# Kernel tuning notes

Measured on AMD Instinct MI355X. Metric: run time of the kernel, lower is better.

The kernel has to match this reference:

```python
import jax, jax.numpy as jnp
import numpy as np

B, T, C, H = 2, 2048, 1024, 16
R = 32
LORA_SCALE = 0.5  # lora_alpha / r = (0.5*rank) / rank
HD = C // H


def setup_inputs() -> dict:
    key = jax.random.key(0)
    ks = jax.random.split(key, 8)
    std = 0.02
    return {
        "x": jax.random.normal(ks[0], (B, T, C), jnp.float32),
        "w_attn": jax.random.normal(ks[1], (3 * C, C), jnp.float32) * std,
        "b_attn": jnp.zeros((3 * C,), jnp.float32),
        "la_attn": jax.random.normal(ks[2], (R, C), jnp.float32) * std,
        "lb_attn": jax.random.normal(ks[3], (3 * C, R), jnp.float32) * std,
        "w_proj": jax.random.normal(ks[4], (C, C), jnp.float32) * std,
        "b_proj": jnp.zeros((C,), jnp.float32),
        "la_proj": jax.random.normal(ks[5], (R, C), jnp.float32) * std,
        "lb_proj": jax.random.normal(ks[6], (C, R), jnp.float32) * std,
    }


def lora_linear(x, w, b, la, lb):
    # y = x @ W^T + b + scale * (x @ A^T) @ B^T
    return x @ w.T + b + LORA_SCALE * ((x @ la.T) @ lb.T)


def reference(x, w_attn, b_attn, la_attn, lb_attn, w_proj, b_proj, la_proj, lb_proj):
    Bsz, Tlen, Cdim = x.shape
    qkv = lora_linear(x, w_attn, b_attn, la_attn, lb_attn)  # [B,T,3C]
    q, k, v = jnp.split(qkv, 3, axis=2)
    # [B,T,C] -> [B,H,T,hd]
    rs = lambda t: t.reshape(Bsz, Tlen, H, HD).transpose(0, 2, 1, 3)
    q, k, v = rs(q), rs(k), rs(v)
    att = jnp.einsum("bhqd,bhkd->bhqk", q, k) * (1.0 / np.sqrt(HD))
    causal = jnp.tril(jnp.ones((Tlen, Tlen), dtype=bool))
    att = jnp.where(causal[None, None], att, -jnp.inf)
    att = jax.nn.softmax(att, axis=-1)
    y = jnp.einsum("bhqk,bhkd->bhqd", att, v)  # [B,H,T,hd]
    y = y.transpose(0, 2, 1, 3).reshape(Bsz, Tlen, Cdim)
    return lora_linear(y, w_proj, b_proj, la_proj, lb_proj)
```

## Files before the change

kernel.cpp:

```cpp
#include <hip/hip_runtime.h>
#include <hip/hip_bf16.h>


typedef __attribute__((ext_vector_type(8))) short short8;
typedef __attribute__((ext_vector_type(4))) float float4v;

static __device__ __forceinline__ float b2f(ushort u) {
  union { uint i; float f; } v; v.i = ((uint)u) << 16; return v.f;
}
static __device__ __forceinline__ ushort f2b(float f) {
  union { float f; uint i; } v; v.f = f;
  uint i = v.i + 0x7fffu + ((v.i >> 16) & 1u);
  return (ushort)(i >> 16);
}
static __device__ __forceinline__ float4v zero4() {
  float4v z = {0.f, 0.f, 0.f, 0.f}; return z;
}
static __device__ __forceinline__ void glld16(const void* g, void* l) {
  __builtin_amdgcn_global_load_lds((const __attribute__((address_space(1))) void*)g,
                                   (__attribute__((address_space(3))) void*)l,
                                   16, 0, 0);
}

__global__ __launch_bounds__(256) void convert_all(
    const float* __restrict__ x, const float* __restrict__ wa,
    const float* __restrict__ la, const float* __restrict__ lb,
    const float* __restrict__ wp, const float* __restrict__ lp,
    const float* __restrict__ lq,
    ushort* __restrict__ xb, ushort* __restrict__ wab, ushort* __restrict__ lab,
    ushort* __restrict__ lbb, ushort* __restrict__ wpb, ushort* __restrict__ lpb,
    ushort* __restrict__ lqb) {
  const int stride = gridDim.x * blockDim.x;
  for (int i = blockIdx.x * blockDim.x + threadIdx.x; i < 2146304; i += stride) {
    const float* s; ushort* d; int off;
    if (i < 1048576)      { s = x;  d = xb;  off = i; }
    else if (i < 1835008) { s = wa; d = wab; off = i - 1048576; }
    else if (i < 1843200) { s = la; d = lab; off = i - 1835008; }
    else if (i < 1867776) { s = lb; d = lbb; off = i - 1843200; }
    else if (i < 2129920) { s = wp; d = wpb; off = i - 1867776; }
    else if (i < 2138112) { s = lp; d = lpb; off = i - 2129920; }
    else                  { s = lq; d = lqb; off = i - 2138112; }
    float4 v = ((const float4*)s)[off];
    union { ushort u[4]; uint2 p; } o;
    o.u[0] = f2b(v.x); o.u[1] = f2b(v.y); o.u[2] = f2b(v.z); o.u[3] = f2b(v.w);
    ((uint2*)d)[off] = o.p;
  }
}

__global__ __launch_bounds__(256) void lora_t(
    const ushort* __restrict__ X, const ushort* __restrict__ La,
    ushort* __restrict__ T) {
  const int tid = threadIdx.x;
  const int m = blockIdx.x * 8 + (tid >> 5);
  const int r = tid & 31;
  const uint4* xr = (const uint4*)(X + (size_t)m * 1024);
  const uint4* lr = (const uint4*)(La + (size_t)r * 1024);
  float s = 0.f;
#pragma unroll 4
  for (int kk = 0; kk < 128; ++kk) {
    uint4 xv = xr[kk], lv = lr[kk];
    s += b2f((ushort)xv.x) * b2f((ushort)lv.x) + b2f((ushort)(xv.x >> 16)) * b2f((ushort)(lv.x >> 16));
    s += b2f((ushort)xv.y) * b2f((ushort)lv.y) + b2f((ushort)(xv.y >> 16)) * b2f((ushort)(lv.y >> 16));
    s += b2f((ushort)xv.z) * b2f((ushort)lv.z) + b2f((ushort)(xv.z >> 16)) * b2f((ushort)(lv.z >> 16));
    s += b2f((ushort)xv.w) * b2f((ushort)lv.w) + b2f((ushort)(xv.w >> 16)) * b2f((ushort)(lv.w >> 16));
  }
  T[(size_t)m * 32 + r] = f2b(0.5f * s);
}

template <bool OUTF32, bool VSPLIT, int NBX>
__global__ __launch_bounds__(256) void gemm_lora(
    const ushort* __restrict__ A, const ushort* __restrict__ W,
    const float* __restrict__ bias,
    const ushort* __restrict__ T1, const ushort* __restrict__ Lb,
    void* __restrict__ outv, ushort* __restrict__ vt, int K, int ldo) {
  __shared__ __attribute__((aligned(16))) ushort As[2][128 * 32];
  __shared__ __attribute__((aligned(16))) ushort Ws[2][128 * 32];
  const int tid = threadIdx.x;
  const int lane = tid & 63, wv = tid >> 6;
  const int l15 = lane & 15, quad = lane >> 4;
  const int L = blockIdx.x;
  const int x8 = L & 7, q = L >> 3;
  const int bx = q % NBX;
  const int by = x8 * 4 + q / NBX;
  const int m0 = by * 128, n0 = bx * 128;
  const int wm = (wv >> 1) * 64, wn = (wv & 1) * 64;
  const int r4 = lane >> 2, c4 = (lane & 3) * 8;
  const int KT = K >> 5;

  float4v acc[4][4];
#pragma unroll
  for (int i = 0; i < 4; i++)
#pragma unroll
    for (int j = 0; j < 4; j++) acc[i][j] = zero4();

  auto stage = [&](int t, int buf) {
    const ushort* sA; const ushort* sW; int ld, k0;
    if (t < KT) { sA = A; sW = W; ld = K; k0 = t * 32; }
    else        { sA = T1; sW = Lb; ld = 32; k0 = 0; }
#pragma unroll
    for (int u = 0; u < 2; ++u) {
      int R = wv * 32 + u * 16;
      glld16(sA + (size_t)(m0 + R + r4) * ld + k0 + c4, &As[buf][R * 32]);
      glld16(sW + (size_t)(n0 + R + r4) * ld + k0 + c4, &Ws[buf][R * 32]);
    }
  };

  stage(0, 0);
  for (int t = 0; t <= KT; ++t) {
    __syncthreads();
    if (t < KT) stage(t + 1, (t + 1) & 1);
    const int b = t & 1;
    short8 af[4], wf[4];
#pragma unroll
    for (int i = 0; i < 4; i++)
      af[i] = *(const short8*)&As[b][(wm + i * 16 + l15) * 32 + quad * 8];
#pragma unroll
    for (int j = 0; j < 4; j++)
      wf[j] = *(const short8*)&Ws[b][(wn + j * 16 + l15) * 32 + quad * 8];
#pragma unroll
    for (int i = 0; i < 4; i++)
#pragma unroll
      for (int j = 0; j < 4; j++)
        acc[i][j] = __builtin_amdgcn_mfma_f32_16x16x32_bf16(af[i], wf[j], acc[i][j], 0, 0, 0);
  }

#pragma unroll
  for (int i = 0; i < 4; i++) {
    int gm = m0 + wm + i * 16 + quad * 4;
#pragma unroll
    for (int j = 0; j < 4; j++) {
      int gn = n0 + wn + j * 16 + l15;
      float bb = bias[gn];
      if (VSPLIT && n0 >= 2048) {
        int vc = gn - 2048;
        int bb2 = gm >> 11, t = gm & 2047;
        ushort u0 = f2b(acc[i][j][0] + bb), u1 = f2b(acc[i][j][1] + bb);
        ushort u2 = f2b(acc[i][j][2] + bb), u3 = f2b(acc[i][j][3] + bb);
        uint2 pk; pk.x = (uint)u0 | ((uint)u1 << 16); pk.y = (uint)u2 | ((uint)u3 << 16);
        *(uint2*)(vt + ((size_t)bb2 * 1024 + vc) * 2048 + t) = pk;
      } else {
#pragma unroll
        for (int r = 0; r < 4; r++) {
          float val = acc[i][j][r] + bb;
          if (OUTF32) ((float*)outv)[(size_t)(gm + r) * ldo + gn] = val;
          else        ((ushort*)outv)[(size_t)(gm + r) * ldo + gn] = f2b(val);
        }
      }
    }
  }
}

__global__ __launch_bounds__(512) void flash_attn(
    const ushort* __restrict__ qk, const ushort* __restrict__ vt,
    ushort* __restrict__ y) {
  __shared__ __attribute__((aligned(16))) ushort Ks[2][64 * 64];
  __shared__ __attribute__((aligned(16))) ushort Vts[2][64 * 64];
  __shared__ __attribute__((aligned(16))) ushort Ps[8 * 16 * 68];
  const int tid = threadIdx.x;
  const int lane = tid & 63, wv = tid >> 6;
  const int l15 = lane & 15, quad = lane >> 4;
  const int bid = blockIdx.x;
  const int idx = bid & 255;
  const int bh = idx & 31;
  const int g = idx >> 5;
  const int qb = (bid < 256) ? (15 - g) : g;
  const int b = bh >> 4, h = bh & 15;
  const ushort* qbase = qk + (size_t)b * 2048 * 2048 + h * 64;
  const ushort* kbase = qk + (size_t)b * 2048 * 2048 + 1024 + h * 64;
  const ushort* vbase = vt + ((size_t)b * 1024 + h * 64) * 2048;
  const int r8 = lane >> 3, c8 = (lane & 7) * 8;

#pragma unroll
  for (int u = 0; u < 2; ++u) {
    int R = wv * 16 + u * 8;
    glld16(qbase + (size_t)(qb * 128 + R + r8) * 2048 + c8, &Ps[R * 64]);
  }
  {
    int R = wv * 8;
    glld16(kbase + (size_t)(R + r8) * 2048 + c8, &Ks[0][R * 64]);
    glld16(vbase + (size_t)(R + r8) * 2048 + c8, &Vts[0][R * 64]);
  }
  __syncthreads();
  short8 aq0 = *(const short8*)&Ps[(wv * 16 + l15) * 64 + quad * 8];
  short8 aq1 = *(const short8*)&Ps[(wv * 16 + l15) * 64 + 32 + quad * 8];
  __syncthreads();

  short8 ones;
#pragma unroll
  for (int e = 0; e < 8; e++) ones[e] = (short)0x3F80;

  float4v acc[4];
#pragma unroll
  for (int jt = 0; jt < 4; jt++) acc[jt] = zero4();
  float4v lacc = zero4();
  const int last = 2 * qb + 1;
  const int qrow0 = qb * 128 + wv * 16;
  const int pB = wv * 16 * 68;

  for (int kb = 0; kb <= last; ++kb) {
    const int cur = kb & 1;
    if (kb < last) {
      const int nb = cur ^ 1;
      const int R = wv * 8;
      glld16(kbase + (size_t)((kb + 1) * 64 + R + r8) * 2048 + c8, &Ks[nb][R * 64]);
      glld16(vbase + (size_t)(R + r8) * 2048 + (kb + 1) * 64 + c8, &Vts[nb][R * 64]);
    }
    float4v s[4];
#pragma unroll
    for (int j = 0; j < 4; ++j) {
      short8 bk0 = *(const short8*)&Ks[cur][(j * 16 + l15) * 64 + quad * 8];
      short8 bk1 = *(const short8*)&Ks[cur][(j * 16 + l15) * 64 + 32 + quad * 8];
      s[j] = zero4();
      s[j] = __builtin_amdgcn_mfma_f32_16x16x32_bf16(aq0, bk0, s[j], 0, 0, 0);
      s[j] = __builtin_amdgcn_mfma_f32_16x16x32_bf16(aq1, bk1, s[j], 0, 0, 0);
    }
    if (kb * 64 + 63 > qrow0) {
#pragma unroll
      for (int j = 0; j < 4; ++j) {
        int key = kb * 64 + j * 16 + l15;
#pragma unroll
        for (int r = 0; r < 4; ++r)
          if (key > qrow0 + quad * 4 + r) s[j][r] = -1e30f;
      }
    }
#pragma unroll
    for (int j = 0; j < 4; ++j)
#pragma unroll
      for (int r = 0; r < 4; ++r) {
        float p = exp2f(s[j][r] * 0.18033688f);
        union { float f; uint i; } u; u.f = p;
        Ps[pB + (quad * 4 + r) * 68 + j * 16 + l15] = (ushort)(u.i >> 16);
      }
#pragma unroll
    for (int kt2 = 0; kt2 < 2; ++kt2) {
      short8 pa = *(const short8*)&Ps[pB + l15 * 68 + kt2 * 32 + quad * 8];
      lacc = __builtin_amdgcn_mfma_f32_16x16x32_bf16(pa, ones, lacc, 0, 0, 0);
#pragma unroll
      for (int jt = 0; jt < 4; ++jt) {
        short8 vb = *(const short8*)&Vts[cur][(jt * 16 + l15) * 64 + kt2 * 32 + quad * 8];
        acc[jt] = __builtin_amdgcn_mfma_f32_16x16x32_bf16(pa, vb, acc[jt], 0, 0, 0);
      }
    }
    __syncthreads();
  }
#pragma unroll
  for (int r = 0; r < 4; ++r) {
    float inv = __builtin_amdgcn_rcpf(lacc[r]);
    int t = qb * 128 + wv * 16 + quad * 4 + r;
#pragma unroll
    for (int jt = 0; jt < 4; ++jt)
      y[(size_t)(b * 2048 + t) * 1024 + h * 64 + jt * 16 + l15] = f2b(acc[jt][r] * inv);
  }
}

extern "C" void kernel_launch(void* const* d_in, const int* in_sizes, int n_in,
                              void* d_out, int out_size, void* d_ws, size_t ws_size,
                              hipStream_t stream) {
  const float* x       = (const float*)d_in[0];
  const float* w_attn  = (const float*)d_in[1];
  const float* b_attn  = (const float*)d_in[2];
  const float* la_attn = (const float*)d_in[3];
  const float* lb_attn = (const float*)d_in[4];
  const float* w_proj  = (const float*)d_in[5];
  const float* b_proj  = (const float*)d_in[6];
  const float* la_proj = (const float*)d_in[7];
  const float* lb_proj = (const float*)d_in[8];

  ushort* p = (ushort*)d_ws;
  ushort* xb   = p; p += (size_t)4096 * 1024;
  ushort* wab  = p; p += (size_t)3072 * 1024;
  ushort* lab  = p; p += (size_t)32 * 1024;
  ushort* lbb  = p; p += (size_t)3072 * 32;
  ushort* wpb  = p; p += (size_t)1024 * 1024;
  ushort* lpb  = p; p += (size_t)32 * 1024;
  ushort* lqb  = p; p += (size_t)1024 * 32;
  ushort* t1b  = p; p += (size_t)4096 * 32;
  ushort* t2b  = p; p += (size_t)4096 * 32;
  ushort* qkb  = p; p += (size_t)4096 * 2048;
  ushort* vtb  = p; p += (size_t)2048 * 2048;
  ushort* yb   = p; p += (size_t)4096 * 1024;

  convert_all<<<dim3(2048), dim3(256), 0, stream>>>(
      x, w_attn, la_attn, lb_attn, w_proj, la_proj, lb_proj,
      xb, wab, lab, lbb, wpb, lpb, lqb);
  lora_t<<<dim3(512), dim3(256), 0, stream>>>(xb, lab, t1b);
  gemm_lora<false, true, 24><<<dim3(768), dim3(256), 0, stream>>>(
      xb, wab, b_attn, t1b, lbb, qkb, vtb, 1024, 2048);
  flash_attn<<<dim3(512), dim3(512), 0, stream>>>(qkb, vtb, yb);
  lora_t<<<dim3(512), dim3(256), 0, stream>>>(yb, lpb, t2b);
  gemm_lora<true, false, 8><<<dim3(256), dim3(256), 0, stream>>>(
      yb, wpb, b_proj, t2b, lqb, d_out, nullptr, 1024, 1024);
}
```

Before: 284.5 us.

## Give each attention wave two query tiles, swizzle LDS, and prescale Q

The flash attention kernel now runs 4 waves per block instead of 8, and each wave handles 32 query rows as two 16-row tiles. Each K and V fragment read from LDS is therefore reused for two MFMAs. Q/K/V tiles are staged with a rotated column swizzle to reduce LDS bank conflicts on fragment reads. The softmax scale (including log2e) is folded into Q in the QKV GEMM epilogue, removing a multiply per score. In exchange each wave holds more accumulators and register pressure rises, and the extra rounding of Q to bf16 after scaling slightly changes numerics.

```diff
diff --git a/kernel.cpp b/kernel.cpp
--- a/kernel.cpp
+++ b/kernel.cpp
@@ -4,6 +4,8 @@
 
 typedef __attribute__((ext_vector_type(8))) short short8;
 typedef __attribute__((ext_vector_type(4))) float float4v;
+
+#define QSCALE 0.18033688011112292f
 
 static __device__ __forceinline__ float b2f(ushort u) {
   union { uint i; float f; } v; v.i = ((uint)u) << 16; return v.f;
@@ -124,6 +126,7 @@
         acc[i][j] = __builtin_amdgcn_mfma_f32_16x16x32_bf16(af[i], wf[j], acc[i][j], 0, 0, 0);
   }
 
+  const float qsc = (VSPLIT && n0 < 1024) ? QSCALE : 1.0f;
 #pragma unroll
   for (int i = 0; i < 4; i++) {
     int gm = m0 + wm + i * 16 + quad * 4;
@@ -141,7 +144,7 @@
       } else {
 #pragma unroll
         for (int r = 0; r < 4; r++) {
-          float val = acc[i][j][r] + bb;
+          float val = (acc[i][j][r] + bb) * qsc;
           if (OUTF32) ((float*)outv)[(size_t)(gm + r) * ldo + gn] = val;
           else        ((ushort*)outv)[(size_t)(gm + r) * ldo + gn] = f2b(val);
         }
@@ -150,12 +153,12 @@
   }
 }
 
-__global__ __launch_bounds__(512) void flash_attn(
+__global__ __launch_bounds__(256) void flash_attn(
     const ushort* __restrict__ qk, const ushort* __restrict__ vt,
     ushort* __restrict__ y) {
   __shared__ __attribute__((aligned(16))) ushort Ks[2][64 * 64];
   __shared__ __attribute__((aligned(16))) ushort Vts[2][64 * 64];
-  __shared__ __attribute__((aligned(16))) ushort Ps[8 * 16 * 68];
+  __shared__ __attribute__((aligned(16))) ushort Ps[4 * 32 * 68];
   const int tid = threadIdx.x;
   const int lane = tid & 63, wv = tid >> 6;
   const int l15 = lane & 15, quad = lane >> 4;
@@ -169,88 +172,125 @@
   const ushort* kbase = qk + (size_t)b * 2048 * 2048 + 1024 + h * 64;
   const ushort* vbase = vt + ((size_t)b * 1024 + h * 64) * 2048;
   const int r8 = lane >> 3, c8 = (lane & 7) * 8;
-
+  const int rotc = (c8 + r8 * 8) & 63;
+  const int colk0 = (quad * 8 + 64 - 8 * (l15 & 7)) & 63;
+  const int colk1 = (colk0 + 32) & 63;
+
+#pragma unroll
+  for (int u = 0; u < 4; ++u) {
+    int R = wv * 32 + u * 8;
+    glld16(qbase + (size_t)(qb * 128 + R + r8) * 2048 + rotc, &Ps[R * 64]);
+  }
 #pragma unroll
   for (int u = 0; u < 2; ++u) {
     int R = wv * 16 + u * 8;
-    glld16(qbase + (size_t)(qb * 128 + R + r8) * 2048 + c8, &Ps[R * 64]);
-  }
-  {
-    int R = wv * 8;
-    glld16(kbase + (size_t)(R + r8) * 2048 + c8, &Ks[0][R * 64]);
-    glld16(vbase + (size_t)(R + r8) * 2048 + c8, &Vts[0][R * 64]);
+    glld16(kbase + (size_t)(R + r8) * 2048 + rotc, &Ks[0][R * 64]);
+    glld16(vbase + (size_t)(R + r8) * 2048 + rotc, &Vts[0][R * 64]);
   }
   __syncthreads();
-  short8 aq0 = *(const short8*)&Ps[(wv * 16 + l15) * 64 + quad * 8];
-  short8 aq1 = *(const short8*)&Ps[(wv * 16 + l15) * 64 + 32 + quad * 8];
+  short8 aq[2][2];
+#pragma unroll
+  for (int i = 0; i < 2; ++i) {
+    const int w = wv * 32 + i * 16 + l15;
+    aq[i][0] = *(const short8*)&Ps[w * 64 + colk0];
+    aq[i][1] = *(const short8*)&Ps[w * 64 + colk1];
+  }
   __syncthreads();
 
   short8 ones;
 #pragma unroll
   for (int e = 0; e < 8; e++) ones[e] = (short)0x3F80;
 
-  float4v acc[4];
-#pragma unroll
-  for (int jt = 0; jt < 4; jt++) acc[jt] = zero4();
-  float4v lacc = zero4();
+  float4v acc[2][4];
+  float4v lacc[2];
+#pragma unroll
+  for (int i = 0; i < 2; ++i) {
+    lacc[i] = zero4();
+#pragma unroll
+    for (int jt = 0; jt < 4; jt++) acc[i][jt] = zero4();
+  }
   const int last = 2 * qb + 1;
-  const int qrow0 = qb * 128 + wv * 16;
-  const int pB = wv * 16 * 68;
+  const int pB = wv * 32 * 68;
 
   for (int kb = 0; kb <= last; ++kb) {
     const int cur = kb & 1;
     if (kb < last) {
       const int nb = cur ^ 1;
-      const int R = wv * 8;
-      glld16(kbase + (size_t)((kb + 1) * 64 + R + r8) * 2048 + c8, &Ks[nb][R * 64]);
-      glld16(vbase + (size_t)(R + r8) * 2048 + (kb + 1) * 64 + c8, &Vts[nb][R * 64]);
-    }
-    float4v s[4];
+#pragma unroll
+      for (int u = 0; u < 2; ++u) {
+        int R = wv * 16 + u * 8;
+        glld16(kbase + (size_t)((kb + 1) * 64 + R + r8) * 2048 + rotc, &Ks[nb][R * 64]);
+        glld16(vbase + (size_t)(R + r8) * 2048 + (kb + 1) * 64 + rotc, &Vts[nb][R * 64]);
+      }
+    }
+    float4v s[2][4];
+#pragma unroll
+    for (int i = 0; i < 2; ++i)
+#pragma unroll
+      for (int j = 0; j < 4; ++j) s[i][j] = zero4();
 #pragma unroll
     for (int j = 0; j < 4; ++j) {
-      short8 bk0 = *(const short8*)&Ks[cur][(j * 16 + l15) * 64 + quad * 8];
-      short8 bk1 = *(const short8*)&Ks[cur][(j * 16 + l15) * 64 + 32 + quad * 8];
-      s[j] = zero4();
-      s[j] = __builtin_amdgcn_mfma_f32_16x16x32_bf16(aq0, bk0, s[j], 0, 0, 0);
-      s[j] = __builtin_amdgcn_mfma_f32_16x16x32_bf16(aq1, bk1, s[j], 0, 0, 0);
-    }
-    if (kb * 64 + 63 > qrow0) {
-#pragma unroll
-      for (int j = 0; j < 4; ++j) {
-        int key = kb * 64 + j * 16 + l15;
-#pragma unroll
-        for (int r = 0; r < 4; ++r)
-          if (key > qrow0 + quad * 4 + r) s[j][r] = -1e30f;
-      }
-    }
-#pragma unroll
-    for (int j = 0; j < 4; ++j)
-#pragma unroll
-      for (int r = 0; r < 4; ++r) {
-        float p = exp2f(s[j][r] * 0.18033688f);
-        union { float f; uint i; } u; u.f = p;
-        Ps[pB + (quad * 4 + r) * 68 + j * 16 + l15] = (ushort)(u.i >> 16);
-      }
+      short8 bk0 = *(const short8*)&Ks[cur][(j * 16 + l15) * 64 + colk0];
+      short8 bk1 = *(const short8*)&Ks[cur][(j * 16 + l15) * 64 + colk1];
+#pragma unroll
+      for (int i = 0; i < 2; ++i) {
+        s[i][j] = __builtin_amdgcn_mfma_f32_16x16x32_bf16(aq[i][0], bk0, s[i][j], 0, 0, 0);
+        s[i][j] = __builtin_amdgcn_mfma_f32_16x16x32_bf16(aq[i][1], bk1, s[i][j], 0, 0, 0);
+      }
+    }
+#pragma unroll
+    for (int i = 0; i < 2; ++i) {
+      const int qrow_i = qb * 128 + wv * 32 + i * 16;
+      if (kb * 64 + 63 > qrow_i) {
+#pragma unroll
+        for (int j = 0; j < 4; ++j) {
+          int key = kb * 64 + j * 16 + l15;
+#pragma unroll
+          for (int r = 0; r < 4; ++r)
+            if (key > qrow_i + quad * 4 + r) s[i][j][r] = -1e30f;
+        }
+      }
+    }
+#pragma unroll
+    for (int i = 0; i < 2; ++i)
+#pragma unroll
+      for (int j = 0; j < 4; ++j)
+#pragma unroll
+        for (int r = 0; r < 4; ++r) {
+          float pv = exp2f(s[i][j][r]);
+          union { float f; uint u; } cv; cv.f = pv;
+          Ps[pB + (i * 16 + quad * 4 + r) * 68 + j * 16 + l15] = (ushort)(cv.u >> 16);
+        }
 #pragma unroll
     for (int kt2 = 0; kt2 < 2; ++kt2) {
-      short8 pa = *(const short8*)&Ps[pB + l15 * 68 + kt2 * 32 + quad * 8];
-      lacc = __builtin_amdgcn_mfma_f32_16x16x32_bf16(pa, ones, lacc, 0, 0, 0);
+      const int vcol = kt2 ? colk1 : colk0;
+      short8 pa[2];
+#pragma unroll
+      for (int i = 0; i < 2; ++i) {
+        pa[i] = *(const short8*)&Ps[pB + (i * 16 + l15) * 68 + kt2 * 32 + quad * 8];
+        lacc[i] = __builtin_amdgcn_mfma_f32_16x16x32_bf16(pa[i], ones, lacc[i], 0, 0, 0);
+      }
 #pragma unroll
       for (int jt = 0; jt < 4; ++jt) {
-        short8 vb = *(const short8*)&Vts[cur][(jt * 16 + l15) * 64 + kt2 * 32 + quad * 8];
-        acc[jt] = __builtin_amdgcn_mfma_f32_16x16x32_bf16(pa, vb, acc[jt], 0, 0, 0);
+        short8 vb = *(const short8*)&Vts[cur][(jt * 16 + l15) * 64 + vcol];
+#pragma unroll
+        for (int i = 0; i < 2; ++i)
+          acc[i][jt] = __builtin_amdgcn_mfma_f32_16x16x32_bf16(pa[i], vb, acc[i][jt], 0, 0, 0);
       }
     }
     __syncthreads();
   }
 #pragma unroll
-  for (int r = 0; r < 4; ++r) {
-    float inv = __builtin_amdgcn_rcpf(lacc[r]);
-    int t = qb * 128 + wv * 16 + quad * 4 + r;
-#pragma unroll
-    for (int jt = 0; jt < 4; ++jt)
-      y[(size_t)(b * 2048 + t) * 1024 + h * 64 + jt * 16 + l15] = f2b(acc[jt][r] * inv);
-  }
+  for (int i = 0; i < 2; ++i)
+#pragma unroll
+    for (int r = 0; r < 4; ++r) {
+      float inv = __builtin_amdgcn_rcpf(lacc[i][r]);
+      int t = qb * 128 + wv * 32 + i * 16 + quad * 4 + r;
+#pragma unroll
+      for (int jt = 0; jt < 4; ++jt)
+        y[(size_t)(b * 2048 + t) * 1024 + h * 64 + jt * 16 + l15] =
+            f2b(acc[i][jt][r] * inv);
+    }
 }
 
 extern "C" void kernel_launch(void* const* d_in, const int* in_sizes, int n_in,
@@ -286,7 +326,7 @@
   lora_t<<<dim3(512), dim3(256), 0, stream>>>(xb, lab, t1b);
   gemm_lora<false, true, 24><<<dim3(768), dim3(256), 0, stream>>>(
       xb, wab, b_attn, t1b, lbb, qkb, vtb, 1024, 2048);
-  flash_attn<<<dim3(512), dim3(512), 0, stream>>>(qkb, vtb, yb);
+  flash_attn<<<dim3(512), dim3(256), 0, stream>>>(qkb, vtb, yb);
   lora_t<<<dim3(512), dim3(256), 0, stream>>>(yb, lpb, t2b);
   gemm_lora<true, false, 8><<<dim3(256), dim3(256), 0, stream>>>(
       yb, wpb, b_proj, t2b, lqb, d_out, nullptr, 1024, 1024);
```

New measurement: 282.2 us. About the same (-0.8%).
